# Optimization experiments

Measured on AMD Instinct MI355X. Metric: run time of the kernel, lower is better.

## Reference

```python
import jax, jax.numpy as jnp
import numpy as np

QLEN, MLEN, BSZ = 1024, 1024, 4
D_MODEL, N_HEAD, D_HEAD = 1024, 16, 64
KLEN = QLEN + MLEN
LN_EPS = 1e-5


def setup_inputs() -> dict:
    key = jax.random.key(0)
    ks = jax.random.split(key, 8)
    w = jax.random.normal(ks[0], (QLEN, BSZ, D_MODEL), jnp.float32)
    mems = jax.random.normal(ks[1], (MLEN, BSZ, D_MODEL), jnp.float32)
    r_emb = jax.random.normal(ks[2], (KLEN, N_HEAD, D_HEAD), jnp.float32) * 0.02
    r_w_bias = jax.random.normal(ks[3], (N_HEAD, D_HEAD), jnp.float32) * 0.02
    r_bias = jax.random.normal(ks[4], (KLEN, N_HEAD), jnp.float32) * 0.02
    Wqkv = jax.random.normal(ks[5], (D_MODEL, 3 * N_HEAD * D_HEAD), jnp.float32) * 0.02
    Wo = jax.random.normal(ks[6], (N_HEAD * D_HEAD, D_MODEL), jnp.float32) * 0.02
    ln_g = jnp.ones((D_MODEL,), jnp.float32)
    ln_b = jnp.zeros((D_MODEL,), jnp.float32)
    # TransfoXL causal mask: query i attends to keys j <= i + mlen
    attn_mask = jnp.triu(jnp.ones((QLEN, KLEN), bool), k=1 + MLEN)
    return {"w": w, "mems": mems, "r_emb": r_emb, "r_w_bias": r_w_bias,
            "r_bias": r_bias, "Wqkv": Wqkv, "Wo": Wo, "ln_g": ln_g,
            "ln_b": ln_b, "attn_mask": attn_mask}


def _rel_shift(x):
    # x: [q, k, b, n] -> TransfoXL relative shift
    q, k, b, n = x.shape
    zero_pad = jnp.zeros((q, 1, b, n), x.dtype)
    x_padded = jnp.concatenate([zero_pad, x], axis=1)  # [q, k+1, b, n]
    x_padded = x_padded.reshape(k + 1, q, b, n)
    return x_padded[1:].reshape(q, k, b, n)


def _layer_norm(x, g, b):
    mu = jnp.mean(x, axis=-1, keepdims=True)
    var = jnp.mean(jnp.square(x - mu), axis=-1, keepdims=True)
    return (x - mu) * jax.lax.rsqrt(var + LN_EPS) * g + b


def reference(w, mems, r_emb, r_w_bias, r_bias, Wqkv, Wo, ln_g, ln_b, attn_mask):
    qlen, bsz = w.shape[0], w.shape[1]
    cat = jnp.concatenate([mems, w], axis=0)            # [klen, b, d]
    klen = cat.shape[0]
    heads = cat @ Wqkv                                  # [klen, b, 3*n*dh]
    hq, hk, hv = jnp.split(heads, 3, axis=-1)
    hq = hq[-qlen:]                                     # [q, b, n*dh]
    q = hq.reshape(qlen, bsz, N_HEAD, D_HEAD)
    k = hk.reshape(klen, bsz, N_HEAD, D_HEAD)
    v = hv.reshape(klen, bsz, N_HEAD, D_HEAD)

    rw_q = q + r_w_bias[None, None]                     # [q, b, n, dh]
    AC = jnp.einsum('ibnd,jbnd->ijbn', rw_q, k)         # [q, k, b, n]
    B_ = jnp.einsum('ibnd,jnd->ijbn', q, r_emb)         # [q, k, b, n]
    BD = _rel_shift(B_ + r_bias[None, :, None, :])
    scale = 1.0 / (D_HEAD ** 0.5)
    attn_score = (AC + BD) * scale

    mask_value = jnp.finfo(attn_score.dtype).min
    attn_score = jnp.where(attn_mask[:, :, None, None], mask_value, attn_score)
    attn_prob = jax.nn.softmax(attn_score, axis=1)

    attn_vec = jnp.einsum('ijbn,jbnd->ibnd', attn_prob, v)
    attn_vec = attn_vec.reshape(qlen, bsz, N_HEAD * D_HEAD)
    attn_out = attn_vec @ Wo
    # post-lnorm residual
    return _layer_norm(w + attn_out, ln_g, ln_b)
```

## Files before the change

kernel.cpp:

```cpp
#include <hip/hip_runtime.h>
#include <hip/hip_bf16.h>
#include <stdint.h>

typedef __attribute__((ext_vector_type(8))) short s16x8;
typedef __attribute__((ext_vector_type(4))) float f32x4;

#define DEVFN static __device__ __forceinline__

DEVFN unsigned short f2bf(float f) {
    union { float f; uint32_t u; } v; v.f = f;
    uint32_t u = v.u;
    uint32_t r = (u + 0x7fffu + ((u >> 16) & 1u)) >> 16;
    return (unsigned short)r;
}
DEVFN float bf2f(unsigned short h) {
    union { uint32_t u; float f; } v; v.u = ((uint32_t)h) << 16;
    return v.f;
}
DEVFN float bfu_lo(uint32_t v) {
    union { uint32_t u; float f; } c; c.u = v << 16; return c.f;
}
DEVFN float bfu_hi(uint32_t v) {
    union { uint32_t u; float f; } c; c.u = v & 0xffff0000u; return c.f;
}
DEVFN uint32_t cvtpk(float lo, float hi) {
    uint32_t r;
    asm("v_cvt_pk_bf16_f32 %0, %1, %2" : "=v"(r) : "v"(lo), "v"(hi));
    return r;
}

DEVFN void gload16(const void* g, void* l) {
    __builtin_amdgcn_global_load_lds(
        (const __attribute__((address_space(1))) unsigned int*)(uintptr_t)g,
        (__attribute__((address_space(3))) unsigned int*)(uint32_t)(uintptr_t)l,
        16, 0, 0);
}

DEVFN f32x4 mfma16(s16x8 a, s16x8 b, f32x4 c) {
    return __builtin_amdgcn_mfma_f32_16x16x32_bf16(a, b, c, 0, 0, 0);
}

DEVFN s16x8 ldfrag(const unsigned short* base, int row, int cb) {
    return *(const s16x8*)((const char*)base + row * 128 + (cb ^ ((row & 7) << 4)));
}

__global__ __launch_bounds__(256) void k_convert_cat(const float* __restrict__ mems,
                                                     const float* __restrict__ w,
                                                     unsigned short* __restrict__ catb) {
    const long long total4 = 2097152;
    for (long long i = (long long)blockIdx.x * blockDim.x + threadIdx.x; i < total4;
         i += (long long)gridDim.x * blockDim.x) {
        float4 v = (i < 1048576) ? ((const float4*)mems)[i] : ((const float4*)w)[i - 1048576];
        ushort4 o = make_ushort4(f2bf(v.x), f2bf(v.y), f2bf(v.z), f2bf(v.w));
        ((ushort4*)catb)[i] = o;
    }
}

__global__ __launch_bounds__(256) void k_transpose_convert(const float* __restrict__ in,
                                                           unsigned short* __restrict__ out,
                                                           int R, int C) {
    __shared__ float T[32][33];
    int c0 = blockIdx.x * 32, r0 = blockIdx.y * 32;
    int tx = threadIdx.x, ty = threadIdx.y;
#pragma unroll
    for (int i = 0; i < 4; ++i) {
        int r = ty * 4 + i;
        T[r][tx] = in[(size_t)(r0 + r) * C + c0 + tx];
    }
    __syncthreads();
#pragma unroll
    for (int i = 0; i < 4; ++i) {
        int r = ty * 4 + i;
        out[(size_t)(c0 + r) * R + r0 + tx] = f2bf(T[tx][r]);
    }
}

__global__ __launch_bounds__(256) void k_remap_remb(const float* __restrict__ r_emb,
                                                    const float* __restrict__ r_bias,
                                                    unsigned short* __restrict__ rb,
                                                    float* __restrict__ rbt) {
    const long long total = 2097152;
    long long tid0 = (long long)blockIdx.x * blockDim.x + threadIdx.x;
    long long stride = (long long)gridDim.x * blockDim.x;
    for (long long o = tid0; o < total; o += stride) {
        int n = (int)(o >> 17);
        int jj = (int)((o >> 6) & 2047);
        int d = (int)(o & 63);
        rb[o] = f2bf(r_emb[((size_t)jj * 16 + n) * 64 + d]);
    }
    for (long long o = tid0; o < 32768; o += stride)
        rbt[o] = r_bias[(size_t)(o & 2047) * 16 + (o >> 11)];
}

__global__ __launch_bounds__(256) void k_vtrans(const unsigned short* __restrict__ vb,
                                                unsigned short* __restrict__ vt) {
    __shared__ unsigned short T[64][72];
    int bn = blockIdx.y;
    int j0 = blockIdx.x * 64;
    int tid = threadIdx.x;
    int r = tid >> 2, cq = (tid & 3) * 16;
    size_t base = (size_t)bn * 131072;
    const unsigned short* src = vb + base + (size_t)(j0 + r) * 64 + cq;
    *(s16x8*)&T[r][cq] = *(const s16x8*)src;
    *(s16x8*)&T[r][cq + 8] = *(const s16x8*)(src + 8);
    __syncthreads();
    int d = r, jq = cq;
    s16x8 o0, o1;
#pragma unroll
    for (int t = 0; t < 8; ++t) { o0[t] = (short)T[jq + t][d]; o1[t] = (short)T[jq + 8 + t][d]; }
    unsigned short* dst = vt + base + (size_t)d * 2048 + j0 + jq;
    *(s16x8*)dst = o0;
    *(s16x8*)(dst + 8) = o1;
}

template <int MODE>
__global__ __launch_bounds__(256) void k_gemm(const unsigned short* __restrict__ A,
                                              const unsigned short* __restrict__ B,
                                              int K, int N,
                                              const float* __restrict__ wres,
                                              float* __restrict__ outf,
                                              unsigned short* __restrict__ qb,
                                              unsigned short* __restrict__ kb,
                                              unsigned short* __restrict__ vb) {
    __shared__ unsigned short As[128 * 64];
    __shared__ unsigned short Bs[128 * 64];
    int tid = threadIdx.x, lane = tid & 63, wid = tid >> 6;
    int l15 = lane & 15, l16 = lane >> 4;
    int m0 = blockIdx.y * 128, n0 = blockIdx.x * 128;
    int wr = wid >> 1, wc = wid & 1;
    f32x4 acc[4][4];
#pragma unroll
    for (int a = 0; a < 4; ++a)
#pragma unroll
        for (int b = 0; b < 4; ++b) acc[a][b] = f32x4{0.f, 0.f, 0.f, 0.f};

    for (int k0 = 0; k0 < K; k0 += 64) {
        __syncthreads();
#pragma unroll
        for (int it = 0; it < 4; ++it) {
            int slot = it * 4 + wid;
            int elem = slot * 512 + lane * 8;
            int row = elem >> 6;
            int colb = (lane & 7) * 16;
            int scol = (colb ^ ((row & 7) << 4)) >> 1;
            gload16(A + (size_t)(m0 + row) * K + k0 + scol, (char*)As + (size_t)slot * 1024);
            gload16(B + (size_t)(n0 + row) * K + k0 + scol, (char*)Bs + (size_t)slot * 1024);
        }
        asm volatile("s_waitcnt vmcnt(0)" ::: "memory");
        __syncthreads();
#pragma unroll
        for (int kc = 0; kc < 2; ++kc) {
            s16x8 af[4], bfr[4];
#pragma unroll
            for (int f = 0; f < 4; ++f)
                af[f] = ldfrag(As, wr * 64 + f * 16 + l15, kc * 64 + l16 * 16);
#pragma unroll
            for (int f = 0; f < 4; ++f)
                bfr[f] = ldfrag(Bs, wc * 64 + f * 16 + l15, kc * 64 + l16 * 16);
#pragma unroll
            for (int fm = 0; fm < 4; ++fm)
#pragma unroll
                for (int fn = 0; fn < 4; ++fn)
                    acc[fm][fn] = mfma16(af[fm], bfr[fn], acc[fm][fn]);
        }
    }
#pragma unroll
    for (int fm = 0; fm < 4; ++fm)
#pragma unroll
        for (int fn = 0; fn < 4; ++fn)
#pragma unroll
            for (int r = 0; r < 4; ++r) {
                int row = m0 + wr * 64 + fm * 16 + l16 * 4 + r;
                int col = n0 + wc * 64 + fn * 16 + l15;
                float v = acc[fm][fn][r];
                if (MODE == 0) {
                    int t = row >> 2, bb = row & 3;
                    if (col < 1024) {
                        if (t >= 1024) {
                            int nn = col >> 6, d = col & 63;
                            qb[((size_t)(bb * 16 + nn) * 1024 + (t - 1024)) * 64 + d] = f2bf(v);
                        }
                    } else if (col < 2048) {
                        int c2 = col - 1024, nn = c2 >> 6, d = c2 & 63;
                        kb[((size_t)(bb * 16 + nn) * 2048 + t) * 64 + d] = f2bf(v);
                    } else {
                        int c2 = col - 2048, nn = c2 >> 6, d = c2 & 63;
                        vb[((size_t)(bb * 16 + nn) * 2048 + t) * 64 + d] = f2bf(v);
                    }
                } else {
                    size_t o = (size_t)row * N + col;
                    outf[o] = v + wres[o];
                }
            }
}

__global__ __launch_bounds__(256) void k_attn(const unsigned short* __restrict__ qb,
                                              const unsigned short* __restrict__ kb,
                                              const unsigned short* __restrict__ vt,
                                              const unsigned short* __restrict__ rb,
                                              const float* __restrict__ rbt,
                                              const float* __restrict__ r_w_bias,
                                              unsigned short* __restrict__ av) {
    __shared__ unsigned short Ks[2][4096];
    __shared__ unsigned short Vs[2][4096];
    __shared__ unsigned short Rs[8192];
    __shared__ unsigned short El[4][1920];
    __shared__ unsigned short Ps[4][1088];
    __shared__ float rbs[128];

    const float SC = 0.18033688f;
    int tid = threadIdx.x, lane = tid & 63, wid = tid >> 6;
    int l15 = lane & 15, l16 = lane >> 4;
    int qr0 = l16 * 4;
    int bn = blockIdx.y, b = bn >> 4, n = bn & 15;
    size_t bq = (size_t)bn * 65536;
    size_t bk = (size_t)bn * 131072;
    int rbase = 48 - wid * 16;
    int lrow = lane >> 3;
    int colb = (lane & 7) * 16;
    int scolE = (colb ^ (lrow << 4)) >> 1;

    unsigned short* ElW = &El[wid][20 * l15 + 21 * qr0];
    const unsigned short* ElR = &El[wid][20 * (l15 + 15) + qr0];
    unsigned short* PsW = &Ps[wid][qr0 * 68 + l15];

    for (int h = 0; h < 2; ++h) {
        int it8 = h ? 15 - (int)blockIdx.x : (int)blockIdx.x;
        int i0 = it8 * 64;
        int njt = it8 + 17;
        int jjb = 960 - i0;

        s16x8 aq[2], aqr[2];
        {
            int qrow = i0 + wid * 16 + l15;
#pragma unroll
            for (int kc = 0; kc < 2; ++kc) {
                s16x8 qv = *(const s16x8*)(qb + bq + (size_t)qrow * 64 + kc * 32 + l16 * 8);
                s16x8 q1, q2;
#pragma unroll
                for (int t = 0; t < 8; ++t) {
                    float f = bf2f((unsigned short)qv[t]);
                    float rw = r_w_bias[n * 64 + kc * 32 + l16 * 8 + t];
                    q1[t] = (short)f2bf(f * SC);
                    q2[t] = (short)f2bf((f + rw) * SC);
                }
                aq[kc] = q1;
                aqr[kc] = q2;
            }
        }

        float m_[4], ls_[4];
        f32x4 accO[4];
#pragma unroll
        for (int r = 0; r < 4; ++r) { m_[r] = -3.0e38f; ls_[r] = 0.f; }
#pragma unroll
        for (int f = 0; f < 4; ++f) accO[f] = f32x4{0.f, 0.f, 0.f, 0.f};

#pragma unroll
        for (int q = 0; q < 2; ++q) {
            int s = wid * 2 + q;
            int row = s * 8 + lrow;
            gload16(kb + bk + (size_t)row * 64 + scolE, (char*)Ks[0] + s * 1024);
            gload16(vt + bk + (size_t)row * 2048 + scolE, (char*)Vs[0] + s * 1024);
        }
#pragma unroll
        for (int q = 0; q < 4; ++q) {
            int s = wid * 4 + q;
            int jju = jjb + s * 8 + lrow;
            int slot8 = (jjb + s * 8) & 127;
            gload16(rb + (size_t)n * 131072 + (size_t)jju * 64 + scolE, (char*)Rs + slot8 * 128);
        }
        if (tid < 128) {
            int jju = jjb + tid;
            rbs[jju & 127] = SC * rbt[(size_t)n * 2048 + jju];
        }
        __syncthreads();

        int cur = 0;
        for (int jt = 0; jt < njt; ++jt) {
            int j0 = jt * 64;
            int jjc = jjb + j0;
            bool pf = (jt + 1 < njt);

            __builtin_amdgcn_s_setprio(1);
#pragma unroll
            for (int fe = 0; fe < 5; ++fe) {
                int slot = (jjc + rbase + fe * 16 + l15) & 127;
                f32x4 e = f32x4{0.f, 0.f, 0.f, 0.f};
                e = mfma16(aq[0], ldfrag(Rs, slot, l16 * 16), e);
                e = mfma16(aq[1], ldfrag(Rs, slot, 64 + l16 * 16), e);
                float rbv = rbs[(jjc + rbase + fe * 16 + l15) & 127];
                uint32_t p01 = cvtpk(e[0] + rbv, e[1] + rbv);
                uint32_t p23 = cvtpk(e[2] + rbv, e[3] + rbv);
                ElW[fe * 320] = (unsigned short)p01;
                ElW[fe * 320 + 21] = (unsigned short)(p01 >> 16);
                ElW[fe * 320 + 42] = (unsigned short)p23;
                ElW[fe * 320 + 63] = (unsigned short)(p23 >> 16);
            }
            f32x4 sAC[4];
#pragma unroll
            for (int fn = 0; fn < 4; ++fn) {
                f32x4 a = f32x4{0.f, 0.f, 0.f, 0.f};
#pragma unroll
                for (int kc = 0; kc < 2; ++kc)
                    a = mfma16(aqr[kc], ldfrag(Ks[cur], fn * 16 + l15, kc * 64 + l16 * 16), a);
                sAC[fn] = a;
            }
            __builtin_amdgcn_s_setprio(0);

            float pe[4][4];
            float lmax[4] = {-3.0e38f, -3.0e38f, -3.0e38f, -3.0e38f};
#pragma unroll
            for (int fn = 0; fn < 4; ++fn) {
                uint2 ev = *(const uint2*)(ElR + fn * 320);
                float e0 = bfu_lo(ev.x), e1 = bfu_hi(ev.x);
                float e2 = bfu_lo(ev.y), e3 = bfu_hi(ev.y);
                pe[fn][0] = sAC[fn][0] + e0;
                pe[fn][1] = sAC[fn][1] + e1;
                pe[fn][2] = sAC[fn][2] + e2;
                pe[fn][3] = sAC[fn][3] + e3;
#pragma unroll
                for (int r = 0; r < 4; ++r) lmax[r] = fmaxf(lmax[r], pe[fn][r]);
            }
            bool need = (lmax[0] > m_[0]) | (lmax[1] > m_[1]) | (lmax[2] > m_[2]) |
                        (lmax[3] > m_[3]);
            if (__any(need)) {
#pragma unroll
                for (int msk = 1; msk <= 8; msk <<= 1)
#pragma unroll
                    for (int r = 0; r < 4; ++r)
                        lmax[r] = fmaxf(lmax[r], __shfl_xor(lmax[r], msk, 64));
#pragma unroll
                for (int r = 0; r < 4; ++r) {
                    float mn = fmaxf(m_[r], lmax[r]);
                    float alpha = __builtin_exp2f(m_[r] - mn);
                    m_[r] = mn;
                    ls_[r] *= alpha;
#pragma unroll
                    for (int f = 0; f < 4; ++f) accO[f][r] *= alpha;
                }
            }
#pragma unroll
            for (int fn = 0; fn < 4; ++fn) {
#pragma unroll
                for (int r = 0; r < 4; ++r) {
                    float e = __builtin_exp2f(pe[fn][r] - m_[r]);
                    pe[fn][r] = e;
                    ls_[r] += e;
                }
                uint32_t a = cvtpk(pe[fn][0], pe[fn][1]);
                uint32_t c = cvtpk(pe[fn][2], pe[fn][3]);
                PsW[fn * 16] = (unsigned short)a;
                PsW[fn * 16 + 68] = (unsigned short)(a >> 16);
                PsW[fn * 16 + 136] = (unsigned short)c;
                PsW[fn * 16 + 204] = (unsigned short)(c >> 16);
            }

            __syncthreads();

            if (pf) {
                int j0n = j0 + 64;
#pragma unroll
                for (int q = 0; q < 2; ++q) {
                    int s = wid * 2 + q;
                    int row = s * 8 + lrow;
                    gload16(kb + bk + (size_t)(j0n + row) * 64 + scolE,
                            (char*)Ks[cur ^ 1] + s * 1024);
                    gload16(vt + bk + (size_t)row * 2048 + j0n + scolE,
                            (char*)Vs[cur ^ 1] + s * 1024);
                }
#pragma unroll
                for (int q = 0; q < 2; ++q) {
                    int s = wid * 2 + q;
                    int jju = jjc + 128 + s * 8 + lrow;
                    int jja = jju > 2047 ? 2047 : jju;
                    int slot8 = (jjc + 128 + s * 8) & 127;
                    gload16(rb + (size_t)n * 131072 + (size_t)jja * 64 + scolE,
                            (char*)Rs + slot8 * 128);
                }
                if (tid < 64) {
                    int jju = jjc + 128 + tid;
                    rbs[jju & 127] = (jju <= 2047) ? SC * rbt[(size_t)n * 2048 + jju] : -1.0e30f;
                }
            }

            __builtin_amdgcn_s_setprio(1);
#pragma unroll
            for (int kc = 0; kc < 2; ++kc) {
                const uint2* pp = (const uint2*)&Ps[wid][l15 * 68 + kc * 32 + l16 * 8];
                union { uint2 u2[2]; s16x8 v; } uu;
                uu.u2[0] = pp[0];
                uu.u2[1] = pp[1];
                s16x8 pa = uu.v;
#pragma unroll
                for (int fd = 0; fd < 4; ++fd)
                    accO[fd] = mfma16(pa, ldfrag(Vs[cur], fd * 16 + l15, kc * 64 + l16 * 16),
                                      accO[fd]);
            }
            __builtin_amdgcn_s_setprio(0);

            __syncthreads();
            cur ^= 1;
        }

#pragma unroll
        for (int msk = 1; msk <= 8; msk <<= 1)
#pragma unroll
            for (int r = 0; r < 4; ++r) ls_[r] += __shfl_xor(ls_[r], msk, 64);

#pragma unroll
        for (int r = 0; r < 4; ++r) {
            float inv = 1.f / ls_[r];
            int ig = i0 + wid * 16 + qr0 + r;
#pragma unroll
            for (int fd = 0; fd < 4; ++fd)
                av[((size_t)ig * 4 + b) * 1024 + n * 64 + fd * 16 + l15] = f2bf(accO[fd][r] * inv);
        }
    }
}

__global__ __launch_bounds__(256) void k_ln(float* __restrict__ y, const float* __restrict__ g,
                                            const float* __restrict__ bta) {
    int row = blockIdx.x, tid = threadIdx.x;
    int lane = tid & 63, wid = tid >> 6;
    float4 v = ((const float4*)(y + (size_t)row * 1024))[tid];
    float s = v.x + v.y + v.z + v.w;
    float sq = v.x * v.x + v.y * v.y + v.z * v.z + v.w * v.w;
#pragma unroll
    for (int msk = 1; msk <= 32; msk <<= 1) {
        s += __shfl_xor(s, msk, 64);
        sq += __shfl_xor(sq, msk, 64);
    }
    __shared__ float red[2][4];
    if (lane == 0) { red[0][wid] = s; red[1][wid] = sq; }
    __syncthreads();
    s = red[0][0] + red[0][1] + red[0][2] + red[0][3];
    sq = red[1][0] + red[1][1] + red[1][2] + red[1][3];
    float mu = s * (1.f / 1024.f);
    float var = sq * (1.f / 1024.f) - mu * mu;
    float rs = rsqrtf(var + 1e-5f);
    float4 gv = ((const float4*)g)[tid];
    float4 bv = ((const float4*)bta)[tid];
    float4 o;
    o.x = (v.x - mu) * rs * gv.x + bv.x;
    o.y = (v.y - mu) * rs * gv.y + bv.y;
    o.z = (v.z - mu) * rs * gv.z + bv.z;
    o.w = (v.w - mu) * rs * gv.w + bv.w;
    ((float4*)(y + (size_t)row * 1024))[tid] = o;
}

extern "C" void kernel_launch(void* const* d_in, const int* in_sizes, int n_in,
                              void* d_out, int out_size, void* d_ws, size_t ws_size,
                              hipStream_t stream) {
    const float* w      = (const float*)d_in[0];
    const float* mems   = (const float*)d_in[1];
    const float* r_emb  = (const float*)d_in[2];
    const float* r_wb   = (const float*)d_in[3];
    const float* r_bias = (const float*)d_in[4];
    const float* Wqkv   = (const float*)d_in[5];
    const float* Wo     = (const float*)d_in[6];
    const float* ln_g   = (const float*)d_in[7];
    const float* ln_b   = (const float*)d_in[8];
    float* out = (float*)d_out;

    char* p = (char*)d_ws;
    auto alloc = [&](size_t bytes) {
        char* q = p;
        p += (bytes + 255) & ~(size_t)255;
        return q;
    };
    unsigned short* catb  = (unsigned short*)alloc(8192ull * 1024 * 2);
    unsigned short* wqkvT = (unsigned short*)alloc(3072ull * 1024 * 2);
    unsigned short* woT   = (unsigned short*)alloc(1024ull * 1024 * 2);
    unsigned short* rb    = (unsigned short*)alloc(16ull * 2048 * 64 * 2);
    float*          rbt   = (float*)alloc(16ull * 2048 * 4);
    unsigned short* qbuf  = (unsigned short*)alloc(64ull * 1024 * 64 * 2);
    unsigned short* kbuf  = (unsigned short*)alloc(64ull * 2048 * 64 * 2);
    unsigned short* vbuf  = (unsigned short*)alloc(64ull * 2048 * 64 * 2);
    unsigned short* av    = (unsigned short*)alloc(4096ull * 1024 * 2);
    unsigned short* vtb = catb;

    k_convert_cat<<<2048, 256, 0, stream>>>(mems, w, catb);
    dim3 tb(32, 8);
    k_transpose_convert<<<dim3(96, 32), tb, 0, stream>>>(Wqkv, wqkvT, 1024, 3072);
    k_transpose_convert<<<dim3(32, 32), tb, 0, stream>>>(Wo, woT, 1024, 1024);
    k_remap_remb<<<2048, 256, 0, stream>>>(r_emb, r_bias, rb, rbt);

    k_gemm<0><<<dim3(24, 64), 256, 0, stream>>>(catb, wqkvT, 1024, 3072, nullptr, nullptr,
                                                qbuf, kbuf, vbuf);
    k_vtrans<<<dim3(32, 64), 256, 0, stream>>>(vbuf, vtb);
    k_attn<<<dim3(8, 64), 256, 0, stream>>>(qbuf, kbuf, vtb, rb, rbt, r_wb, av);
    k_gemm<1><<<dim3(8, 32), 256, 0, stream>>>(av, woT, 1024, 1024, w, out,
                                               nullptr, nullptr, nullptr);
    k_ln<<<4096, 256, 0, stream>>>(out, ln_g, ln_b);
}
```

Measured before the change: 266.1 us.

## Skip unused Q projection rows, merge prep kernels, triple-buffer R and fold row sums into MFMA

The QKV GEMM is split into two launches so that Q columns are computed only for the last qlen rows (mems rows never need Q), which drops about a sixth of the projection work. The r_emb remap is merged into the input conversion kernel to save a launch. In attention, the R tile becomes a 192-row ring buffer so the K/V/R prefetch can be issued before the softmax and one __syncthreads per tile can be removed. The softmax row sum is accumulated with an MFMA against a ones vector, replacing the scalar adds and the final shuffle reduction. The probability buffer now shares LDS with the E buffer, which cuts LDS use but relies on the intra-warp write and read order being correct.

```diff
diff --git a/kernel.cpp b/kernel.cpp
--- a/kernel.cpp
+++ b/kernel.cpp
@@ -44,16 +44,28 @@
     return *(const s16x8*)((const char*)base + row * 128 + (cb ^ ((row & 7) << 4)));
 }
 
-__global__ __launch_bounds__(256) void k_convert_cat(const float* __restrict__ mems,
-                                                     const float* __restrict__ w,
-                                                     unsigned short* __restrict__ catb) {
-    const long long total4 = 2097152;
-    for (long long i = (long long)blockIdx.x * blockDim.x + threadIdx.x; i < total4;
-         i += (long long)gridDim.x * blockDim.x) {
+__global__ __launch_bounds__(256) void k_prep(const float* __restrict__ mems,
+                                              const float* __restrict__ w,
+                                              const float* __restrict__ r_emb,
+                                              const float* __restrict__ r_bias,
+                                              unsigned short* __restrict__ catb,
+                                              unsigned short* __restrict__ rb,
+                                              float* __restrict__ rbt) {
+    long long tid0 = (long long)blockIdx.x * blockDim.x + threadIdx.x;
+    long long stride = (long long)gridDim.x * blockDim.x;
+    for (long long i = tid0; i < 2097152; i += stride) {
         float4 v = (i < 1048576) ? ((const float4*)mems)[i] : ((const float4*)w)[i - 1048576];
         ushort4 o = make_ushort4(f2bf(v.x), f2bf(v.y), f2bf(v.z), f2bf(v.w));
         ((ushort4*)catb)[i] = o;
     }
+    for (long long o = tid0; o < 2097152; o += stride) {
+        int n = (int)(o >> 17);
+        int jj = (int)((o >> 6) & 2047);
+        int d = (int)(o & 63);
+        rb[o] = f2bf(r_emb[((size_t)jj * 16 + n) * 64 + d]);
+    }
+    for (long long o = tid0; o < 32768; o += stride)
+        rbt[o] = r_bias[(size_t)(o & 2047) * 16 + (o >> 11)];
 }
 
 __global__ __launch_bounds__(256) void k_transpose_convert(const float* __restrict__ in,
@@ -73,23 +85,6 @@
         int r = ty * 4 + i;
         out[(size_t)(c0 + r) * R + r0 + tx] = f2bf(T[tx][r]);
     }
-}
-
-__global__ __launch_bounds__(256) void k_remap_remb(const float* __restrict__ r_emb,
-                                                    const float* __restrict__ r_bias,
-                                                    unsigned short* __restrict__ rb,
-                                                    float* __restrict__ rbt) {
-    const long long total = 2097152;
-    long long tid0 = (long long)blockIdx.x * blockDim.x + threadIdx.x;
-    long long stride = (long long)gridDim.x * blockDim.x;
-    for (long long o = tid0; o < total; o += stride) {
-        int n = (int)(o >> 17);
-        int jj = (int)((o >> 6) & 2047);
-        int d = (int)(o & 63);
-        rb[o] = f2bf(r_emb[((size_t)jj * 16 + n) * 64 + d]);
-    }
-    for (long long o = tid0; o < 32768; o += stride)
-        rbt[o] = r_bias[(size_t)(o & 2047) * 16 + (o >> 11)];
 }
 
 __global__ __launch_bounds__(256) void k_vtrans(const unsigned short* __restrict__ vb,
@@ -116,7 +111,7 @@
 template <int MODE>
 __global__ __launch_bounds__(256) void k_gemm(const unsigned short* __restrict__ A,
                                               const unsigned short* __restrict__ B,
-                                              int K, int N,
+                                              int K, int N, int m_base, int n_base,
                                               const float* __restrict__ wres,
                                               float* __restrict__ outf,
                                               unsigned short* __restrict__ qb,
@@ -126,7 +121,7 @@
     __shared__ unsigned short Bs[128 * 64];
     int tid = threadIdx.x, lane = tid & 63, wid = tid >> 6;
     int l15 = lane & 15, l16 = lane >> 4;
-    int m0 = blockIdx.y * 128, n0 = blockIdx.x * 128;
+    int m0 = m_base + blockIdx.y * 128, n0 = n_base + blockIdx.x * 128;
     int wr = wid >> 1, wc = wid & 1;
     f32x4 acc[4][4];
 #pragma unroll
@@ -203,10 +198,9 @@
                                               unsigned short* __restrict__ av) {
     __shared__ unsigned short Ks[2][4096];
     __shared__ unsigned short Vs[2][4096];
-    __shared__ unsigned short Rs[8192];
-    __shared__ unsigned short El[4][1920];
-    __shared__ unsigned short Ps[4][1088];
-    __shared__ float rbs[128];
+    __shared__ unsigned short Rs[192 * 64];
+    __shared__ unsigned short Elp[4][1920];
+    __shared__ float rbs[192];
 
     const float SC = 0.18033688f;
     int tid = threadIdx.x, lane = tid & 63, wid = tid >> 6;
@@ -220,9 +214,14 @@
     int colb = (lane & 7) * 16;
     int scolE = (colb ^ (lrow << 4)) >> 1;
 
-    unsigned short* ElW = &El[wid][20 * l15 + 21 * qr0];
-    const unsigned short* ElR = &El[wid][20 * (l15 + 15) + qr0];
-    unsigned short* PsW = &Ps[wid][qr0 * 68 + l15];
+    unsigned short* ElW = &Elp[wid][20 * l15 + 21 * qr0];
+    const unsigned short* ElR = &Elp[wid][20 * (l15 + 15) + qr0];
+    unsigned short* PsW = &Elp[wid][qr0 * 68 + l15];
+    const unsigned short* PsR = &Elp[wid][l15 * 68];
+
+    s16x8 ones;
+#pragma unroll
+    for (int t = 0; t < 8; ++t) ones[t] = (short)0x3F80;
 
     for (int h = 0; h < 2; ++h) {
         int it8 = h ? 15 - (int)blockIdx.x : (int)blockIdx.x;
@@ -249,12 +248,13 @@
             }
         }
 
-        float m_[4], ls_[4];
-        f32x4 accO[4];
-#pragma unroll
-        for (int r = 0; r < 4; ++r) { m_[r] = -3.0e38f; ls_[r] = 0.f; }
+        float m_[4];
+        f32x4 accO[4], accL;
+#pragma unroll
+        for (int r = 0; r < 4; ++r) m_[r] = -3.0e38f;
 #pragma unroll
         for (int f = 0; f < 4; ++f) accO[f] = f32x4{0.f, 0.f, 0.f, 0.f};
+        accL = f32x4{0.f, 0.f, 0.f, 0.f};
 
 #pragma unroll
         for (int q = 0; q < 2; ++q) {
@@ -267,16 +267,16 @@
         for (int q = 0; q < 4; ++q) {
             int s = wid * 4 + q;
             int jju = jjb + s * 8 + lrow;
-            int slot8 = (jjb + s * 8) & 127;
-            gload16(rb + (size_t)n * 131072 + (size_t)jju * 64 + scolE, (char*)Rs + slot8 * 128);
+            gload16(rb + (size_t)n * 131072 + (size_t)jju * 64 + scolE,
+                    (char*)Rs + (s * 8) * 128);
         }
         if (tid < 128) {
             int jju = jjb + tid;
-            rbs[jju & 127] = SC * rbt[(size_t)n * 2048 + jju];
+            rbs[tid] = SC * rbt[(size_t)n * 2048 + jju];
         }
         __syncthreads();
 
-        int cur = 0;
+        int cur = 0, rsb = 0;
         for (int jt = 0; jt < njt; ++jt) {
             int j0 = jt * 64;
             int jjc = jjb + j0;
@@ -285,11 +285,12 @@
             __builtin_amdgcn_s_setprio(1);
 #pragma unroll
             for (int fe = 0; fe < 5; ++fe) {
-                int slot = (jjc + rbase + fe * 16 + l15) & 127;
+                int row = rsb + rbase + fe * 16 + l15;
+                if (row >= 192) row -= 192;
                 f32x4 e = f32x4{0.f, 0.f, 0.f, 0.f};
-                e = mfma16(aq[0], ldfrag(Rs, slot, l16 * 16), e);
-                e = mfma16(aq[1], ldfrag(Rs, slot, 64 + l16 * 16), e);
-                float rbv = rbs[(jjc + rbase + fe * 16 + l15) & 127];
+                e = mfma16(aq[0], ldfrag(Rs, row, l16 * 16), e);
+                e = mfma16(aq[1], ldfrag(Rs, row, 64 + l16 * 16), e);
+                float rbv = rbs[row];
                 uint32_t p01 = cvtpk(e[0] + rbv, e[1] + rbv);
                 uint32_t p23 = cvtpk(e[2] + rbv, e[3] + rbv);
                 ElW[fe * 320] = (unsigned short)p01;
@@ -307,6 +308,35 @@
                 sAC[fn] = a;
             }
             __builtin_amdgcn_s_setprio(0);
+
+            if (pf) {
+                int j0n = j0 + 64;
+#pragma unroll
+                for (int q = 0; q < 2; ++q) {
+                    int s = wid * 2 + q;
+                    int row = s * 8 + lrow;
+                    gload16(kb + bk + (size_t)(j0n + row) * 64 + scolE,
+                            (char*)Ks[cur ^ 1] + s * 1024);
+                    gload16(vt + bk + (size_t)row * 2048 + j0n + scolE,
+                            (char*)Vs[cur ^ 1] + s * 1024);
+                }
+#pragma unroll
+                for (int q = 0; q < 2; ++q) {
+                    int s = wid * 2 + q;
+                    int w = rsb + 128 + s * 8;
+                    if (w >= 192) w -= 192;
+                    int jju = jjc + 128 + s * 8 + lrow;
+                    int jja = jju > 2047 ? 2047 : jju;
+                    gload16(rb + (size_t)n * 131072 + (size_t)jja * 64 + scolE,
+                            (char*)Rs + w * 128);
+                }
+                if (tid < 64) {
+                    int w = rsb + 128 + tid;
+                    if (w >= 192) w -= 192;
+                    int jju = jjc + 128 + tid;
+                    rbs[w] = (jju <= 2047) ? SC * rbt[(size_t)n * 2048 + jju] : -1.0e30f;
+                }
+            }
 
             float pe[4][4];
             float lmax[4] = {-3.0e38f, -3.0e38f, -3.0e38f, -3.0e38f};
@@ -335,63 +365,34 @@
                     float mn = fmaxf(m_[r], lmax[r]);
                     float alpha = __builtin_exp2f(m_[r] - mn);
                     m_[r] = mn;
-                    ls_[r] *= alpha;
+                    accL[r] *= alpha;
 #pragma unroll
                     for (int f = 0; f < 4; ++f) accO[f][r] *= alpha;
                 }
             }
 #pragma unroll
             for (int fn = 0; fn < 4; ++fn) {
-#pragma unroll
-                for (int r = 0; r < 4; ++r) {
-                    float e = __builtin_exp2f(pe[fn][r] - m_[r]);
-                    pe[fn][r] = e;
-                    ls_[r] += e;
-                }
-                uint32_t a = cvtpk(pe[fn][0], pe[fn][1]);
-                uint32_t c = cvtpk(pe[fn][2], pe[fn][3]);
+                float e0 = __builtin_exp2f(pe[fn][0] - m_[0]);
+                float e1 = __builtin_exp2f(pe[fn][1] - m_[1]);
+                float e2 = __builtin_exp2f(pe[fn][2] - m_[2]);
+                float e3 = __builtin_exp2f(pe[fn][3] - m_[3]);
+                uint32_t a = cvtpk(e0, e1);
+                uint32_t c = cvtpk(e2, e3);
                 PsW[fn * 16] = (unsigned short)a;
                 PsW[fn * 16 + 68] = (unsigned short)(a >> 16);
                 PsW[fn * 16 + 136] = (unsigned short)c;
                 PsW[fn * 16 + 204] = (unsigned short)(c >> 16);
             }
 
-            __syncthreads();
-
-            if (pf) {
-                int j0n = j0 + 64;
-#pragma unroll
-                for (int q = 0; q < 2; ++q) {
-                    int s = wid * 2 + q;
-                    int row = s * 8 + lrow;
-                    gload16(kb + bk + (size_t)(j0n + row) * 64 + scolE,
-                            (char*)Ks[cur ^ 1] + s * 1024);
-                    gload16(vt + bk + (size_t)row * 2048 + j0n + scolE,
-                            (char*)Vs[cur ^ 1] + s * 1024);
-                }
-#pragma unroll
-                for (int q = 0; q < 2; ++q) {
-                    int s = wid * 2 + q;
-                    int jju = jjc + 128 + s * 8 + lrow;
-                    int jja = jju > 2047 ? 2047 : jju;
-                    int slot8 = (jjc + 128 + s * 8) & 127;
-                    gload16(rb + (size_t)n * 131072 + (size_t)jja * 64 + scolE,
-                            (char*)Rs + slot8 * 128);
-                }
-                if (tid < 64) {
-                    int jju = jjc + 128 + tid;
-                    rbs[jju & 127] = (jju <= 2047) ? SC * rbt[(size_t)n * 2048 + jju] : -1.0e30f;
-                }
-            }
-
             __builtin_amdgcn_s_setprio(1);
 #pragma unroll
             for (int kc = 0; kc < 2; ++kc) {
-                const uint2* pp = (const uint2*)&Ps[wid][l15 * 68 + kc * 32 + l16 * 8];
+                const uint2* pp = (const uint2*)(PsR + kc * 32 + l16 * 8);
                 union { uint2 u2[2]; s16x8 v; } uu;
                 uu.u2[0] = pp[0];
                 uu.u2[1] = pp[1];
                 s16x8 pa = uu.v;
+                accL = mfma16(pa, ones, accL);
 #pragma unroll
                 for (int fd = 0; fd < 4; ++fd)
                     accO[fd] = mfma16(pa, ldfrag(Vs[cur], fd * 16 + l15, kc * 64 + l16 * 16),
@@ -401,16 +402,13 @@
 
             __syncthreads();
             cur ^= 1;
-        }
-
-#pragma unroll
-        for (int msk = 1; msk <= 8; msk <<= 1)
-#pragma unroll
-            for (int r = 0; r < 4; ++r) ls_[r] += __shfl_xor(ls_[r], msk, 64);
+            rsb += 64;
+            if (rsb == 192) rsb = 0;
+        }
 
 #pragma unroll
         for (int r = 0; r < 4; ++r) {
-            float inv = 1.f / ls_[r];
+            float inv = 1.f / accL[r];
             int ig = i0 + wid * 16 + qr0 + r;
 #pragma unroll
             for (int fd = 0; fd < 4; ++fd)
@@ -480,17 +478,18 @@
     unsigned short* av    = (unsigned short*)alloc(4096ull * 1024 * 2);
     unsigned short* vtb = catb;
 
-    k_convert_cat<<<2048, 256, 0, stream>>>(mems, w, catb);
+    k_prep<<<2048, 256, 0, stream>>>(mems, w, r_emb, r_bias, catb, rb, rbt);
     dim3 tb(32, 8);
     k_transpose_convert<<<dim3(96, 32), tb, 0, stream>>>(Wqkv, wqkvT, 1024, 3072);
     k_transpose_convert<<<dim3(32, 32), tb, 0, stream>>>(Wo, woT, 1024, 1024);
-    k_remap_remb<<<2048, 256, 0, stream>>>(r_emb, r_bias, rb, rbt);
-
-    k_gemm<0><<<dim3(24, 64), 256, 0, stream>>>(catb, wqkvT, 1024, 3072, nullptr, nullptr,
-                                                qbuf, kbuf, vbuf);
+
+    k_gemm<0><<<dim3(16, 64), 256, 0, stream>>>(catb, wqkvT, 1024, 3072, 0, 1024,
+                                                nullptr, nullptr, qbuf, kbuf, vbuf);
+    k_gemm<0><<<dim3(8, 32), 256, 0, stream>>>(catb, wqkvT, 1024, 3072, 4096, 0,
+                                               nullptr, nullptr, qbuf, kbuf, vbuf);
     k_vtrans<<<dim3(32, 64), 256, 0, stream>>>(vbuf, vtb);
     k_attn<<<dim3(8, 64), 256, 0, stream>>>(qbuf, kbuf, vtb, rb, rbt, r_wb, av);
-    k_gemm<1><<<dim3(8, 32), 256, 0, stream>>>(av, woT, 1024, 1024, w, out,
-                                               nullptr, nullptr, nullptr);
+    k_gemm<1><<<dim3(8, 32), 256, 0, stream>>>(av, woT, 1024, 1024, 0, 0,
+                                               w, out, nullptr, nullptr, nullptr);
     k_ln<<<4096, 256, 0, stream>>>(out, ln_g, ln_b);
 }
```

Result: slower. 284.5 us (+6.9%).
